# Kernel optimization log

Measured on AMD Instinct MI355X. Metric: run time of the kernel, lower is better.

## Reference

```python
import jax, jax.numpy as jnp
import numpy as np

SPARSITY = 0.5  # cur_sparsity set during training; 0.0 default would make masking a no-op
WEIGHT_BETA = 1.0
MASK_ALPHA1 = 1.0
MASK_ALPHA2 = 1.0


def binarize(mask_scores, sparsity):
    # SparseBinarizer.forward: prune (set to 0) the `num_prune` smallest scores globally.
    num_prune = int(mask_scores.size * sparsity)  # static: sparsity is a Python float
    flat = mask_scores.reshape(-1)
    prune_idx = jnp.argsort(flat)[:num_prune]
    mask = jnp.ones_like(flat).at[prune_idx].set(0.0)
    return mask.reshape(mask_scores.shape)


def setup_inputs() -> dict:
    key = jax.random.key(0)
    ks = jax.random.split(key, 9)
    out_f, in_f, r = 4096, 4096, 8
    tokens = 8192  # batch 4 * seq 2048
    return {
        "x": jax.random.normal(ks[0], (tokens, in_f), dtype=jnp.float32),
        "weight": jax.random.normal(ks[1], (out_f, in_f), dtype=jnp.float32) * 0.02,
        "bias": jax.random.normal(ks[2], (out_f,), dtype=jnp.float32) * 0.02,
        "weight_U": jax.random.normal(ks[3], (out_f, r), dtype=jnp.float32),
        "weight_V": jnp.zeros((r, in_f), dtype=jnp.float32),
        "mask_scores_A": jax.random.normal(ks[4], (out_f, r), dtype=jnp.float32),
        "mask_scores_B": jnp.zeros((r, in_f), dtype=jnp.float32),
        "mask_scores_R": jnp.zeros((out_f,), dtype=jnp.float32),
        "mask_scores_C": jnp.zeros((in_f,), dtype=jnp.float32),
    }


def reference(x, weight, bias, weight_U, weight_V, mask_scores_A, mask_scores_B,
              mask_scores_R, mask_scores_C):
    # weight = W + beta * U @ V   (low-rank weight reconstruction)
    w = weight + WEIGHT_BETA * (weight_U @ weight_V)
    # mask_scores = |w| + a1 * A @ B + a2 * (R[:,None] + C[None,:])
    mask_scores = (jnp.abs(w)
                   + MASK_ALPHA1 * (mask_scores_A @ mask_scores_B)
                   + MASK_ALPHA2 * (mask_scores_R[:, None] + mask_scores_C[None, :]))
    mask = binarize(mask_scores, SPARSITY)
    masked_weight = mask * w  # [out_f, in_f]
    # nn.Linear: x @ W^T + b
    return x @ masked_weight.T + bias
```

## Files before the change

kernel.cpp:

```cpp
#include <hip/hip_runtime.h>
#include <stdint.h>

#define TOKENS 8192
#define OUT_F  4096
#define IN_F   4096
#define RNK    8
#define RPB    4
#define KPRUNE 8388608u
#define CAP3   16384u

typedef unsigned short u16;
typedef float  f32x4  __attribute__((ext_vector_type(4)));
typedef short  bf16x8 __attribute__((ext_vector_type(8)));
typedef unsigned short u16x4 __attribute__((ext_vector_type(4)));
typedef unsigned short u16x8 __attribute__((ext_vector_type(8)));

#define XB_OFF    0ull
#define WB_OFF    67108864ull
#define KEYS_OFF  100663296ull
#define CTL_OFF   167772160ull
#define H1_OFF    0
#define H2_OFF    16384
#define SEL_OFF   32768
#define CNT3_OFF  32800
#define LIST3_OFF 32804
#define CTL_ZERO_U32 8201

__device__ __forceinline__ u16 f2bf(float f) {
    uint32_t u = __float_as_uint(f);
    u += 0x7fffu + ((u >> 16) & 1u);
    return (u16)(u >> 16);
}

__device__ __forceinline__ uint32_t fkey(float s) {
    uint32_t u = __float_as_uint(s);
    return (u & 0x80000000u) ? ~u : (u | 0x80000000u);
}

__global__ void convx_kernel(const float* __restrict__ x, u16* __restrict__ xB,
                             uint32_t* __restrict__ ctl)
{
    const int t = threadIdx.x;
    if (blockIdx.x < 34) {
        const int i = blockIdx.x * 256 + t;
        if (i < CTL_ZERO_U32) ctl[i] = 0u;
    }
    const size_t idx = (size_t)blockIdx.x * 256 + t;
    const float4* xv = (const float4*)x;
    float4 a = xv[idx*2];
    float4 b = xv[idx*2 + 1];
    u16x8 o;
    o[0]=f2bf(a.x); o[1]=f2bf(a.y); o[2]=f2bf(a.z); o[3]=f2bf(a.w);
    o[4]=f2bf(b.x); o[5]=f2bf(b.y); o[6]=f2bf(b.z); o[7]=f2bf(b.w);
    *((u16x8*)xB + idx) = o;
}

__global__ void prep_kernel(const float* __restrict__ W, const float* __restrict__ U,
                            const float* __restrict__ V, const float* __restrict__ A,
                            const float* __restrict__ B, const float* __restrict__ R,
                            const float* __restrict__ C, u16* __restrict__ wB,
                            uint32_t* __restrict__ keys, uint32_t* __restrict__ hist1)
{
    __shared__ uint32_t lh[2][4096];
    const int o0 = blockIdx.x * RPB, t = threadIdx.x;
    uint32_t* lhs = lh[t & 1];
    for (int b = t; b < 8192; b += 256) ((uint32_t*)lh)[b] = 0u;
    float uu[RPB][RNK], aa[RPB][RNK], ro[RPB];
#pragma unroll
    for (int r0 = 0; r0 < RPB; ++r0) {
#pragma unroll
        for (int r = 0; r < RNK; ++r) {
            uu[r0][r] = U[(o0+r0)*RNK + r];
            aa[r0][r] = A[(o0+r0)*RNK + r];
        }
        ro[r0] = R[o0 + r0];
    }
    __syncthreads();
    for (int j = 0; j < IN_F/1024; ++j) {
        const int i = j*1024 + t*4;
        const float4 cc = *(const float4*)&C[i];
#pragma unroll
        for (int r0 = 0; r0 < RPB; ++r0) {
            float4 wv = *(const float4*)&W[(size_t)(o0+r0)*IN_F + i];
#pragma unroll
            for (int r = 0; r < RNK; ++r) {
                const float4 v4 = *(const float4*)&V[r*IN_F + i];
                const float u0 = uu[r0][r];
                wv.x = fmaf(u0, v4.x, wv.x); wv.y = fmaf(u0, v4.y, wv.y);
                wv.z = fmaf(u0, v4.z, wv.z); wv.w = fmaf(u0, v4.w, wv.w);
            }
            float4 s;
            s.x = fabsf(wv.x); s.y = fabsf(wv.y); s.z = fabsf(wv.z); s.w = fabsf(wv.w);
#pragma unroll
            for (int r = 0; r < RNK; ++r) {
                const float4 b4 = *(const float4*)&B[r*IN_F + i];
                const float a0 = aa[r0][r];
                s.x = fmaf(a0, b4.x, s.x); s.y = fmaf(a0, b4.y, s.y);
                s.z = fmaf(a0, b4.z, s.z); s.w = fmaf(a0, b4.w, s.w);
            }
            const float rr = ro[r0];
            s.x += rr + cc.x; s.y += rr + cc.y; s.z += rr + cc.z; s.w += rr + cc.w;
            uint4 k4;
            k4.x = fkey(s.x); k4.y = fkey(s.y); k4.z = fkey(s.z); k4.w = fkey(s.w);
            *(uint4*)&keys[(size_t)(o0+r0)*IN_F + i] = k4;
            u16x4 w4;
            w4[0] = f2bf(wv.x); w4[1] = f2bf(wv.y); w4[2] = f2bf(wv.z); w4[3] = f2bf(wv.w);
            *(u16x4*)&wB[(size_t)(o0+r0)*IN_F + i] = w4;
            atomicAdd(&lhs[k4.x >> 20], 1u);
            atomicAdd(&lhs[k4.y >> 20], 1u);
            atomicAdd(&lhs[k4.z >> 20], 1u);
            atomicAdd(&lhs[k4.w >> 20], 1u);
        }
    }
    __syncthreads();
    for (int b = t; b < 4096; b += 256) {
        const uint32_t c = lh[0][b] + lh[1][b];
        if (c) atomicAdd(&hist1[b], c);
    }
}

__global__ void select_kernel(const uint32_t* __restrict__ hist, uint32_t* sel, int mode)
{
    __shared__ uint32_t lh[4096];
    __shared__ uint32_t part[256];
    __shared__ uint32_t sseg[2];
    const int t = threadIdx.x;
    const uint32_t c1v = sel[1];
    const uint32_t k = (mode == 0) ? KPRUNE : (KPRUNE - c1v);
    for (int b = t; b < 4096; b += 256) lh[b] = hist[b];
    __syncthreads();
    uint32_t s = 0;
    for (int j = 0; j < 16; ++j) s += lh[t*16 + j];
    part[t] = s;
    __syncthreads();
    uint32_t pre = 0;
    for (int tt = 0; tt < t; ++tt) pre += part[tt];
    if (pre < k && pre + part[t] >= k) { sseg[0] = (uint32_t)t; sseg[1] = pre; }
    __syncthreads();
    const int seg = (int)sseg[0];
    const uint32_t accb = sseg[1];
    if (t < 16) {
        uint32_t pre2 = 0;
        for (int j = 0; j < t; ++j) pre2 += lh[seg*16 + j];
        const uint32_t c = lh[seg*16 + t];
        const uint32_t below = accb + pre2;
        if (below < k && below + c >= k) {
            const uint32_t bin = (uint32_t)(seg*16 + t);
            if (mode == 0) { sel[0] = bin; sel[1] = below; }
            else           { sel[2] = bin; sel[3] = c1v + below; }
        }
    }
}

__global__ void hist2_kernel(const uint32_t* __restrict__ keys, const uint32_t* __restrict__ sel,
                             uint32_t* __restrict__ hist2)
{
    __shared__ uint32_t lh[4096];
    const int o = blockIdx.x, t = threadIdx.x;
    const uint32_t b1 = sel[0];
    for (int b = t; b < 4096; b += 256) lh[b] = 0u;
    __syncthreads();
    const uint32_t* kp = keys + (size_t)o*IN_F + t*16;
#pragma unroll
    for (int q = 0; q < 4; ++q) {
        uint4 kv = *(const uint4*)(kp + q*4);
        if ((kv.x >> 20) == b1) atomicAdd(&lh[(kv.x >> 8) & 0xFFFu], 1u);
        if ((kv.y >> 20) == b1) atomicAdd(&lh[(kv.y >> 8) & 0xFFFu], 1u);
        if ((kv.z >> 20) == b1) atomicAdd(&lh[(kv.z >> 8) & 0xFFFu], 1u);
        if ((kv.w >> 20) == b1) atomicAdd(&lh[(kv.w >> 8) & 0xFFFu], 1u);
    }
    __syncthreads();
    for (int b = t; b < 4096; b += 256) { uint32_t c = lh[b]; if (c) atomicAdd(&hist2[b], c); }
}

__global__ void collect3_kernel(const uint32_t* __restrict__ keys, const uint32_t* __restrict__ sel,
                                uint32_t* __restrict__ cnt3, uint32_t* __restrict__ list3)
{
    const uint32_t pfx = (sel[0] << 12) | sel[2];
    const size_t base = ((size_t)blockIdx.x * 256 + threadIdx.x) * 16;
#pragma unroll
    for (int q = 0; q < 4; ++q) {
        uint4 kv = *(const uint4*)(keys + base + q*4);
        const uint32_t i0 = (uint32_t)(base + q*4);
        if ((kv.x >> 8) == pfx) { uint32_t s = atomicAdd(cnt3, 1u); if (s < CAP3) list3[s] = ((i0+0u) << 8) | (kv.x & 0xFFu); }
        if ((kv.y >> 8) == pfx) { uint32_t s = atomicAdd(cnt3, 1u); if (s < CAP3) list3[s] = ((i0+1u) << 8) | (kv.y & 0xFFu); }
        if ((kv.z >> 8) == pfx) { uint32_t s = atomicAdd(cnt3, 1u); if (s < CAP3) list3[s] = ((i0+2u) << 8) | (kv.z & 0xFFu); }
        if ((kv.w >> 8) == pfx) { uint32_t s = atomicAdd(cnt3, 1u); if (s < CAP3) list3[s] = ((i0+3u) << 8) | (kv.w & 0xFFu); }
    }
}

__global__ void selfix_kernel(uint32_t* sel, const uint32_t* __restrict__ cnt3,
                              const uint32_t* __restrict__ list3, u16* __restrict__ wB)
{
    __shared__ uint32_t lst[CAP3];
    __shared__ uint32_t hist[256];
    __shared__ uint32_t sv[2];
    const int t = threadIdx.x;
    uint32_t n = *cnt3; if (n > CAP3) n = CAP3;
    hist[t] = 0u;
    __syncthreads();
    for (uint32_t i = t; i < n; i += 256) {
        const uint32_t e = list3[i];
        lst[i] = e;
        atomicAdd(&hist[e & 0xFFu], 1u);
    }
    __syncthreads();
    const uint32_t k3 = KPRUNE - sel[3];
    uint32_t pre = 0;
    for (int b = 0; b < t; ++b) pre += hist[b];
    if (pre < k3 && pre + hist[t] >= k3) {
        sv[0] = (uint32_t)t;
        sv[1] = k3 - pre;
        sel[4] = (sel[0] << 20) | (sel[2] << 8) | (uint32_t)t;
    }
    __syncthreads();
    const uint32_t b3 = sv[0], p = sv[1];
    for (uint32_t i = t; i < n; i += 256) {
        const uint32_t e = lst[i];
        if ((e & 0xFFu) != b3) continue;
        uint32_t rank = 0;
        for (uint32_t j = 0; j < n; ++j) {
            const uint32_t f = lst[j];
            rank += ((f & 0xFFu) == b3 && f < e) ? 1u : 0u;
        }
        if (rank < p) wB[e >> 8] = 0u;
    }
}

__global__ void apply_kernel(const uint32_t* __restrict__ keys, const uint32_t* __restrict__ sel,
                             u16* __restrict__ wB)
{
    const uint32_t thr = sel[4];
    const size_t base = ((size_t)blockIdx.x * 256 + threadIdx.x) * 16;
    uint32_t kv[16];
#pragma unroll
    for (int q = 0; q < 4; ++q) *(uint4*)(kv + q*4) = *(const uint4*)(keys + base + q*4);
    uint4 wraw[2];
    wraw[0] = *(const uint4*)(wB + base);
    wraw[1] = *(const uint4*)(wB + base + 8);
    u16* wv = (u16*)wraw;
#pragma unroll
    for (int e = 0; e < 16; ++e) if (kv[e] < thr) wv[e] = 0u;
    *(uint4*)(wB + base)     = wraw[0];
    *(uint4*)(wB + base + 8) = wraw[1];
}

#define LA0 0
#define LB0 32768
#define LA1 65536
#define LB1 98304

__device__ __forceinline__ void gl_lds16(const char* src, char* dst) {
    __builtin_amdgcn_global_load_lds((const __attribute__((address_space(1))) void*)src,
                                     (__attribute__((address_space(3))) void*)dst, 16, 0, 0);
}

__global__ __launch_bounds__(512, 2) void gemm256_kernel(const u16* __restrict__ xB,
                                                         const u16* __restrict__ wB,
                                                         const float* __restrict__ bias,
                                                         float* __restrict__ out)
{
    __shared__ char ldsc[131072];
    const int t    = threadIdx.x;
    const int lane = t & 63;
    const int wid  = t >> 6;
    const int wm   = wid >> 2;
    const int wn   = wid & 3;
    const int orig = blockIdx.x;
    const int tid  = (orig & 7) * 64 + (orig >> 3);
    const int bn   = tid >> 5;
    const int bm   = tid & 31;

    const int l15 = lane & 15;
    const int kb  = (lane >> 4) << 4;
    const int sw  = (lane & 7) << 4;
    const int bA  = (16*wm + l15) * 128 + kb;
    const int bB  = (64*wn + l15) * 128 + kb;

    const int scol = ((t & 7) * 16) ^ (((t >> 3) & 7) << 4);
    const char* pA = (const char*)xB + ((size_t)(bm*256 + (t >> 3))) * (IN_F*2) + scol;
    const char* pB = (const char*)wB + ((size_t)(bn*256 + (t >> 3))) * (IN_F*2) + scol;
    const int tb16 = t * 16;

#define STAGE(pG, reg, h, tile) do {                                          \
    const char* _s = (pG) + (size_t)(tile)*128 + (size_t)(h)*(128*IN_F*2);    \
    char* _d = ldsc + (reg) + (h)*16384 + tb16;                               \
    gl_lds16(_s, _d);                                                         \
    gl_lds16(_s + (size_t)(64*IN_F*2), _d + 8192);                            \
} while (0)

    f32x4  acc[8][4] = {};
    bf16x8 b[4][2];
    bf16x8 a[2][2];

#define LOADB(reg) do {                                                       \
    _Pragma("unroll") for (int ni = 0; ni < 4; ++ni)                          \
    _Pragma("unroll") for (int kk = 0; kk < 2; ++kk)                          \
        b[ni][kk] = *(const bf16x8*)(ldsc + (reg) +                           \
                      ((bB + ni*2048 + kk*64) ^ sw));                         \
} while (0)

#define LOADA(reg, q) do {                                                    \
    _Pragma("unroll") for (int mm = 0; mm < 2; ++mm)                          \
    _Pragma("unroll") for (int kk = 0; kk < 2; ++kk)                          \
        a[mm][kk] = *(const bf16x8*)(ldsc + (reg) +                           \
                      ((bA + (2*(q)+mm)*4096 + kk*64) ^ sw));                 \
} while (0)

#define MFMAQ(q) do {                                                         \
    _Pragma("unroll") for (int mm = 0; mm < 2; ++mm)                          \
    _Pragma("unroll") for (int ni = 0; ni < 4; ++ni)                          \
    _Pragma("unroll") for (int kk = 0; kk < 2; ++kk)                          \
        acc[2*(q)+mm][ni] = __builtin_amdgcn_mfma_f32_16x16x32_bf16(          \
            a[mm][kk], b[ni][kk], acc[2*(q)+mm][ni], 0, 0, 0);                \
} while (0)

#define PH_TAIL(q)                                                            \
    __builtin_amdgcn_s_barrier();                                             \
    asm volatile("s_waitcnt lgkmcnt(0)" ::: "memory");                        \
    __builtin_amdgcn_s_setprio(1);                                            \
    MFMAQ(q);                                                                 \
    __builtin_amdgcn_s_setprio(0);                                            \
    __builtin_amdgcn_s_barrier();

    STAGE(pB, LB0, 0, 0);
    STAGE(pB, LB0, 1, 0);
    STAGE(pA, LA0, 0, 0);
    STAGE(pA, LA0, 1, 0);
    STAGE(pB, LB1, 0, 1);
    STAGE(pB, LB1, 1, 1);
    STAGE(pA, LA1, 0, 1);
    asm volatile("s_waitcnt vmcnt(6)" ::: "memory");
    __builtin_amdgcn_s_barrier();

#pragma unroll 1
    for (int j = 0; j < IN_F/64/2; ++j) {
        const int to = 2*j + 1;
        const int se = (2*j + 2) & 63;
        const int so = (2*j + 3) & 63;

        LOADB(LB0); LOADA(LA0, 0);
        STAGE(pA, LA1, 1, to);
        asm volatile("s_waitcnt lgkmcnt(8)" ::: "memory");
        PH_TAIL(0)
        LOADA(LA0, 1);
        STAGE(pB, LB0, 0, se);
        PH_TAIL(1)
        LOADA(LA0, 2);
        STAGE(pB, LB0, 1, se);
        PH_TAIL(2)
        LOADA(LA0, 3);
        STAGE(pA, LA0, 0, se);
        asm volatile("s_waitcnt vmcnt(6)" ::: "memory");
        PH_TAIL(3)

        LOADB(LB1); LOADA(LA1, 0);
        STAGE(pA, LA0, 1, se);
        asm volatile("s_waitcnt lgkmcnt(8)" ::: "memory");
        PH_TAIL(0)
        LOADA(LA1, 1);
        STAGE(pB, LB1, 0, so);
        PH_TAIL(1)
        LOADA(LA1, 2);
        STAGE(pB, LB1, 1, so);
        PH_TAIL(2)
        LOADA(LA1, 3);
        STAGE(pA, LA1, 0, so);
        asm volatile("s_waitcnt vmcnt(6)" ::: "memory");
        PH_TAIL(3)
    }

    const int orow0 = bm*256 + 16*wm + ((lane >> 4) << 2);
    const int ocol0 = bn*256 + 64*wn + l15;
#pragma unroll
    for (int ni = 0; ni < 4; ++ni) {
        const int col = ocol0 + ni*16;
        const float bv = bias[col];
#pragma unroll
        for (int m = 0; m < 8; ++m) {
            const int r0 = orow0 + 32*m;
            f32x4 v = acc[m][ni];
#pragma unroll
            for (int q = 0; q < 4; ++q)
                out[(size_t)(r0 + q)*OUT_F + col] = v[q] + bv;
        }
    }
#undef STAGE
#undef LOADB
#undef LOADA
#undef MFMAQ
#undef PH_TAIL
}

extern "C" void kernel_launch(void* const* d_in, const int* in_sizes, int n_in,
                              void* d_out, int out_size, void* d_ws, size_t ws_size,
                              hipStream_t stream)
{
    const float* x    = (const float*)d_in[0];
    const float* W    = (const float*)d_in[1];
    const float* bias = (const float*)d_in[2];
    const float* U    = (const float*)d_in[3];
    const float* V    = (const float*)d_in[4];
    const float* A    = (const float*)d_in[5];
    const float* B    = (const float*)d_in[6];
    const float* R    = (const float*)d_in[7];
    const float* C    = (const float*)d_in[8];
    float* out = (float*)d_out;

    char* ws = (char*)d_ws;
    u16*      xB    = (u16*)(ws + XB_OFF);
    u16*      wB    = (u16*)(ws + WB_OFF);
    uint32_t* keys  = (uint32_t*)(ws + KEYS_OFF);
    uint32_t* ctl   = (uint32_t*)(ws + CTL_OFF);
    uint32_t* h1    = (uint32_t*)((char*)ctl + H1_OFF);
    uint32_t* h2    = (uint32_t*)((char*)ctl + H2_OFF);
    uint32_t* sel   = (uint32_t*)((char*)ctl + SEL_OFF);
    uint32_t* cnt3  = (uint32_t*)((char*)ctl + CNT3_OFF);
    uint32_t* list3 = (uint32_t*)((char*)ctl + LIST3_OFF);

    convx_kernel<<<TOKENS*IN_F/8/256, 256, 0, stream>>>(x, xB, ctl);
    prep_kernel<<<OUT_F/RPB, 256, 0, stream>>>(W, U, V, A, B, R, C, wB, keys, h1);
    select_kernel<<<1, 256, 0, stream>>>(h1, sel, 0);
    hist2_kernel<<<OUT_F, 256, 0, stream>>>(keys, sel, h2);
    select_kernel<<<1, 256, 0, stream>>>(h2, sel, 1);
    collect3_kernel<<<OUT_F, 256, 0, stream>>>(keys, sel, cnt3, list3);
    selfix_kernel<<<1, 256, 0, stream>>>(sel, cnt3, list3, wB);
    apply_kernel<<<OUT_F, 256, 0, stream>>>(keys, sel, wB);
    gemm256_kernel<<<(TOKENS/256)*(OUT_F/256), 512, 0, stream>>>(xB, wB, bias, out);
}
```

Before: 459.1 us.

## Fuse collect and apply passes, scalarize prep, simplify GEMM tile order

Merges the level-3 candidate collection into the mask-apply kernel, so keys are read once. Elements below the bucket prefix are zeroed directly and boundary-bucket elements are finished in selfix, which removes one full pass over the 64 MB key array. The prep kernel moves from float4 to scalar per-thread processing with a single shared histogram instead of two interleaved copies. The GEMM drops its swizzled block-to-tile mapping for a plain row-major order and writes output with nontemporal stores; the simpler tile order may reduce L2 reuse.

After: 411.1 us. 10.4% less time.

```diff
diff --git a/kernel.cpp b/kernel.cpp
--- a/kernel.cpp
+++ b/kernel.cpp
@@ -12,7 +12,6 @@
 typedef unsigned short u16;
 typedef float  f32x4  __attribute__((ext_vector_type(4)));
 typedef short  bf16x8 __attribute__((ext_vector_type(8)));
-typedef unsigned short u16x4 __attribute__((ext_vector_type(4)));
 typedef unsigned short u16x8 __attribute__((ext_vector_type(8)));
 
 #define XB_OFF    0ull
@@ -61,10 +60,9 @@
                             const float* __restrict__ C, u16* __restrict__ wB,
                             uint32_t* __restrict__ keys, uint32_t* __restrict__ hist1)
 {
-    __shared__ uint32_t lh[2][4096];
+    __shared__ uint32_t lh[4096];
     const int o0 = blockIdx.x * RPB, t = threadIdx.x;
-    uint32_t* lhs = lh[t & 1];
-    for (int b = t; b < 8192; b += 256) ((uint32_t*)lh)[b] = 0u;
+    for (int b = t; b < 4096; b += 256) lh[b] = 0u;
     float uu[RPB][RNK], aa[RPB][RNK], ro[RPB];
 #pragma unroll
     for (int r0 = 0; r0 < RPB; ++r0) {
@@ -76,47 +74,29 @@
         ro[r0] = R[o0 + r0];
     }
     __syncthreads();
-    for (int j = 0; j < IN_F/1024; ++j) {
-        const int i = j*1024 + t*4;
-        const float4 cc = *(const float4*)&C[i];
+    for (int j = 0; j < IN_F/256; ++j) {
+        const int i = j*256 + t;
+        float vv[RNK], bb[RNK];
+#pragma unroll
+        for (int r = 0; r < RNK; ++r) { vv[r] = V[r*IN_F + i]; bb[r] = B[r*IN_F + i]; }
+        const float ci = C[i];
 #pragma unroll
         for (int r0 = 0; r0 < RPB; ++r0) {
-            float4 wv = *(const float4*)&W[(size_t)(o0+r0)*IN_F + i];
-#pragma unroll
-            for (int r = 0; r < RNK; ++r) {
-                const float4 v4 = *(const float4*)&V[r*IN_F + i];
-                const float u0 = uu[r0][r];
-                wv.x = fmaf(u0, v4.x, wv.x); wv.y = fmaf(u0, v4.y, wv.y);
-                wv.z = fmaf(u0, v4.z, wv.z); wv.w = fmaf(u0, v4.w, wv.w);
-            }
-            float4 s;
-            s.x = fabsf(wv.x); s.y = fabsf(wv.y); s.z = fabsf(wv.z); s.w = fabsf(wv.w);
-#pragma unroll
-            for (int r = 0; r < RNK; ++r) {
-                const float4 b4 = *(const float4*)&B[r*IN_F + i];
-                const float a0 = aa[r0][r];
-                s.x = fmaf(a0, b4.x, s.x); s.y = fmaf(a0, b4.y, s.y);
-                s.z = fmaf(a0, b4.z, s.z); s.w = fmaf(a0, b4.w, s.w);
-            }
-            const float rr = ro[r0];
-            s.x += rr + cc.x; s.y += rr + cc.y; s.z += rr + cc.z; s.w += rr + cc.w;
-            uint4 k4;
-            k4.x = fkey(s.x); k4.y = fkey(s.y); k4.z = fkey(s.z); k4.w = fkey(s.w);
-            *(uint4*)&keys[(size_t)(o0+r0)*IN_F + i] = k4;
-            u16x4 w4;
-            w4[0] = f2bf(wv.x); w4[1] = f2bf(wv.y); w4[2] = f2bf(wv.z); w4[3] = f2bf(wv.w);
-            *(u16x4*)&wB[(size_t)(o0+r0)*IN_F + i] = w4;
-            atomicAdd(&lhs[k4.x >> 20], 1u);
-            atomicAdd(&lhs[k4.y >> 20], 1u);
-            atomicAdd(&lhs[k4.z >> 20], 1u);
-            atomicAdd(&lhs[k4.w >> 20], 1u);
-        }
-    }
-    __syncthreads();
-    for (int b = t; b < 4096; b += 256) {
-        const uint32_t c = lh[0][b] + lh[1][b];
-        if (c) atomicAdd(&hist1[b], c);
-    }
+            float wv = W[(size_t)(o0+r0)*IN_F + i];
+#pragma unroll
+            for (int r = 0; r < RNK; ++r) wv = fmaf(uu[r0][r], vv[r], wv);
+            float s = fabsf(wv);
+#pragma unroll
+            for (int r = 0; r < RNK; ++r) s = fmaf(aa[r0][r], bb[r], s);
+            s += ro[r0] + ci;
+            const uint32_t key = fkey(s);
+            keys[(size_t)(o0+r0)*IN_F + i] = key;
+            wB[(size_t)(o0+r0)*IN_F + i]   = f2bf(wv);
+            atomicAdd(&lh[key >> 20], 1u);
+        }
+    }
+    __syncthreads();
+    for (int b = t; b < 4096; b += 256) { uint32_t c = lh[b]; if (c) atomicAdd(&hist1[b], c); }
 }
 
 __global__ void select_kernel(const uint32_t* __restrict__ hist, uint32_t* sel, int mode)
@@ -173,23 +153,33 @@
     for (int b = t; b < 4096; b += 256) { uint32_t c = lh[b]; if (c) atomicAdd(&hist2[b], c); }
 }
 
-__global__ void collect3_kernel(const uint32_t* __restrict__ keys, const uint32_t* __restrict__ sel,
-                                uint32_t* __restrict__ cnt3, uint32_t* __restrict__ list3)
+__global__ void apply_kernel(const uint32_t* __restrict__ keys, const uint32_t* __restrict__ sel,
+                             u16* __restrict__ wB, uint32_t* __restrict__ cnt3,
+                             uint32_t* __restrict__ list3)
 {
     const uint32_t pfx = (sel[0] << 12) | sel[2];
     const size_t base = ((size_t)blockIdx.x * 256 + threadIdx.x) * 16;
-#pragma unroll
-    for (int q = 0; q < 4; ++q) {
-        uint4 kv = *(const uint4*)(keys + base + q*4);
-        const uint32_t i0 = (uint32_t)(base + q*4);
-        if ((kv.x >> 8) == pfx) { uint32_t s = atomicAdd(cnt3, 1u); if (s < CAP3) list3[s] = ((i0+0u) << 8) | (kv.x & 0xFFu); }
-        if ((kv.y >> 8) == pfx) { uint32_t s = atomicAdd(cnt3, 1u); if (s < CAP3) list3[s] = ((i0+1u) << 8) | (kv.y & 0xFFu); }
-        if ((kv.z >> 8) == pfx) { uint32_t s = atomicAdd(cnt3, 1u); if (s < CAP3) list3[s] = ((i0+2u) << 8) | (kv.z & 0xFFu); }
-        if ((kv.w >> 8) == pfx) { uint32_t s = atomicAdd(cnt3, 1u); if (s < CAP3) list3[s] = ((i0+3u) << 8) | (kv.w & 0xFFu); }
-    }
-}
-
-__global__ void selfix_kernel(uint32_t* sel, const uint32_t* __restrict__ cnt3,
+    uint32_t kv[16];
+#pragma unroll
+    for (int q = 0; q < 4; ++q) *(uint4*)(kv + q*4) = *(const uint4*)(keys + base + q*4);
+    uint4 wraw[2];
+    wraw[0] = *(const uint4*)(wB + base);
+    wraw[1] = *(const uint4*)(wB + base + 8);
+    u16* wv = (u16*)wraw;
+#pragma unroll
+    for (int e = 0; e < 16; ++e) {
+        const uint32_t hi = kv[e] >> 8;
+        if (hi < pfx) wv[e] = 0u;
+        else if (hi == pfx) {
+            uint32_t s = atomicAdd(cnt3, 1u);
+            if (s < CAP3) list3[s] = ((uint32_t)(base + e) << 8) | (kv[e] & 0xFFu);
+        }
+    }
+    *(uint4*)(wB + base)     = wraw[0];
+    *(uint4*)(wB + base + 8) = wraw[1];
+}
+
+__global__ void selfix_kernel(const uint32_t* __restrict__ sel, const uint32_t* __restrict__ cnt3,
                               const uint32_t* __restrict__ list3, u16* __restrict__ wB)
 {
     __shared__ uint32_t lst[CAP3];
@@ -211,13 +201,14 @@
     if (pre < k3 && pre + hist[t] >= k3) {
         sv[0] = (uint32_t)t;
         sv[1] = k3 - pre;
-        sel[4] = (sel[0] << 20) | (sel[2] << 8) | (uint32_t)t;
     }
     __syncthreads();
     const uint32_t b3 = sv[0], p = sv[1];
     for (uint32_t i = t; i < n; i += 256) {
         const uint32_t e = lst[i];
-        if ((e & 0xFFu) != b3) continue;
+        const uint32_t lo = e & 0xFFu;
+        if (lo < b3) { wB[e >> 8] = 0u; continue; }
+        if (lo != b3) continue;
         uint32_t rank = 0;
         for (uint32_t j = 0; j < n; ++j) {
             const uint32_t f = lst[j];
@@ -225,24 +216,6 @@
         }
         if (rank < p) wB[e >> 8] = 0u;
     }
-}
-
-__global__ void apply_kernel(const uint32_t* __restrict__ keys, const uint32_t* __restrict__ sel,
-                             u16* __restrict__ wB)
-{
-    const uint32_t thr = sel[4];
-    const size_t base = ((size_t)blockIdx.x * 256 + threadIdx.x) * 16;
-    uint32_t kv[16];
-#pragma unroll
-    for (int q = 0; q < 4; ++q) *(uint4*)(kv + q*4) = *(const uint4*)(keys + base + q*4);
-    uint4 wraw[2];
-    wraw[0] = *(const uint4*)(wB + base);
-    wraw[1] = *(const uint4*)(wB + base + 8);
-    u16* wv = (u16*)wraw;
-#pragma unroll
-    for (int e = 0; e < 16; ++e) if (kv[e] < thr) wv[e] = 0u;
-    *(uint4*)(wB + base)     = wraw[0];
-    *(uint4*)(wB + base + 8) = wraw[1];
 }
 
 #define LA0 0
@@ -266,10 +239,9 @@
     const int wid  = t >> 6;
     const int wm   = wid >> 2;
     const int wn   = wid & 3;
-    const int orig = blockIdx.x;
-    const int tid  = (orig & 7) * 64 + (orig >> 3);
-    const int bn   = tid >> 5;
-    const int bm   = tid & 31;
+    const int bid  = blockIdx.x;
+    const int bn   = bid & 15;
+    const int bm   = bid >> 4;
 
     const int l15 = lane & 15;
     const int kb  = (lane >> 4) << 4;
@@ -382,7 +354,7 @@
             f32x4 v = acc[m][ni];
 #pragma unroll
             for (int q = 0; q < 4; ++q)
-                out[(size_t)(r0 + q)*OUT_F + col] = v[q] + bv;
+                __builtin_nontemporal_store(v[q] + bv, &out[(size_t)(r0 + q)*OUT_F + col]);
         }
     }
 #undef STAGE
@@ -423,8 +395,7 @@
     select_kernel<<<1, 256, 0, stream>>>(h1, sel, 0);
     hist2_kernel<<<OUT_F, 256, 0, stream>>>(keys, sel, h2);
     select_kernel<<<1, 256, 0, stream>>>(h2, sel, 1);
-    collect3_kernel<<<OUT_F, 256, 0, stream>>>(keys, sel, cnt3, list3);
+    apply_kernel<<<OUT_F, 256, 0, stream>>>(keys, sel, wB, cnt3, list3);
     selfix_kernel<<<1, 256, 0, stream>>>(sel, cnt3, list3, wB);
-    apply_kernel<<<OUT_F, 256, 0, stream>>>(keys, sel, wB);
     gemm256_kernel<<<(TOKENS/256)*(OUT_F/256), 512, 0, stream>>>(xB, wB, bias, out);
 }
```
